# Kernel optimization log

Measured on AMD Instinct MI355X. Metric: run time of the kernel, lower is better.

## Reference

```python
import jax, jax.numpy as jnp
from jax import lax
import numpy as np

HIDDEN = 1024
FEAT = 512
PREV = 10
PRED = 20
BATCH = 1024


def setup_inputs() -> dict:
    key = jax.random.key(0)
    ks = jax.random.split(key, 12)
    s_in = 1.0 / np.sqrt(FEAT)
    s_h = 1.0 / np.sqrt(HIDDEN)
    return {
        "real_input": jax.random.normal(ks[0], (BATCH, PREV + PRED, FEAT), jnp.float32),
        "fake_input": jax.random.normal(ks[1], (BATCH, PRED, FEAT), jnp.float32),
        "Wx": jax.random.normal(ks[2], (FEAT, 4 * HIDDEN), jnp.float32) * s_in,
        "Wh": jax.random.normal(ks[3], (HIDDEN, 4 * HIDDEN), jnp.float32) * s_h,
        "b": jnp.zeros((4 * HIDDEN,), jnp.float32),
        "w2": jax.random.normal(ks[4], (HIDDEN, 1), jnp.float32) * s_h,
        "b2": jnp.zeros((1,), jnp.float32),
        "w3": jax.random.normal(ks[5], (1, 1), jnp.float32),
        "b3": jnp.zeros((1,), jnp.float32),
        "w4": jax.random.normal(ks[6], (1, 1), jnp.float32),
        "b4": jnp.zeros((1,), jnp.float32),
    }


def _lstm_hidden_states(seq, Wx, Wh, b):
    # seq: [B, T, F] -> hidden states hs: [T, B, H]
    B = seq.shape[0]
    xz = jnp.einsum("btf,fk->btk", seq, Wx) + b  # precompute input projections

    def step(carry, xz_t):
        h, c = carry
        z = xz_t + h @ Wh  # [B, 4H]
        i, f, g, o = jnp.split(z, 4, axis=-1)
        i = jax.nn.sigmoid(i)
        f = jax.nn.sigmoid(f)
        g = jnp.tanh(g)
        o = jax.nn.sigmoid(o)
        c = f * c + i * g
        h = o * jnp.tanh(c)
        return (h, c), h

    h0 = jnp.zeros((B, Wh.shape[0]), seq.dtype)
    _, hs = lax.scan(step, (h0, h0), jnp.swapaxes(xz, 0, 1))
    return hs


def _dense_chain(h, w2, b2, w3, b3, w4, b4):
    x = jnp.tanh(h @ w2 + b2)
    x = jnp.tanh(x @ w3 + b3)
    x = jnp.tanh(x @ w4 + b4)
    return x


def reference(real_input, fake_input, Wx, Wh, b, w2, b2, w3, b3, w4, b4):
    # trajectory_real[k] is the prefix real_input[:, :PREV+k+1]; running the
    # LSTM from zero state over each prefix equals taking hidden state at
    # step PREV+k of a single scan over the full sequence.
    fake_seq = jnp.concatenate([real_input[:, :PREV, :], fake_input], axis=1)

    hs_real = _lstm_hidden_states(real_input, Wx, Wh, b)[PREV:PREV + PRED]  # [PRED,B,H]
    hs_fake = _lstm_hidden_states(fake_seq, Wx, Wh, b)[PREV:PREV + PRED]

    real_pred = _dense_chain(hs_real, w2, b2, w3, b3, w4, b4)  # [PRED,B,1]
    fake_pred = _dense_chain(hs_fake, w2, b2, w3, b3, w4, b4)

    real_pred = jnp.swapaxes(real_pred, 0, 1)  # [B,PRED,1]
    fake_pred = jnp.swapaxes(fake_pred, 0, 1)
    return real_pred, fake_pred
```

## Files before the change

kernel.cpp:

```cpp
#include <hip/hip_runtime.h>
#include <hip/hip_bf16.h>
#include <stdint.h>
#include <string.h>

#define HIDDEN 1024
#define FEAT   512
#define PREV   10
#define PRED   20
#define BATCH  1024
#define KTOT   (HIDDEN + FEAT)
#define N4H    4096
#define TSTEPS (PREV + PRED)
#define NBLK   256
#define NTHR   512
#define NKT    24
#define TILEB  16384

typedef __attribute__((ext_vector_type(8))) short short8;
typedef __attribute__((ext_vector_type(4))) float f32x4;
typedef unsigned long long ull;

typedef __attribute__((address_space(3))) unsigned int u32_lds;
typedef const __attribute__((address_space(1))) unsigned int u32_gbl;

__device__ __forceinline__ void async16(void* lds, const void* g) {
  u32_lds* lp = (u32_lds*)(unsigned int)(uintptr_t)lds;
  u32_gbl* gp = (u32_gbl*)(uintptr_t)g;
  __builtin_amdgcn_global_load_lds(gp, lp, 16, 0, 0);
}

__device__ __forceinline__ float sigmoidf_(float x) {
  return 1.0f / (1.0f + __expf(-x));
}
__device__ __forceinline__ float tanhf_(float x) {
  return 1.0f - 2.0f / (1.0f + __expf(2.0f * x));
}

__device__ __forceinline__ ull cload(const void* p) {
  return __hip_atomic_load((const ull*)p, __ATOMIC_RELAXED, __HIP_MEMORY_SCOPE_AGENT);
}
__device__ __forceinline__ void cstore(void* p, ull v) {
  __hip_atomic_store((ull*)p, v, __ATOMIC_RELAXED, __HIP_MEMORY_SCOPE_AGENT);
}
__device__ __forceinline__ float cload4(const void* p) {
  return __hip_atomic_load((const float*)p, __ATOMIC_RELAXED, __HIP_MEMORY_SCOPE_AGENT);
}
__device__ __forceinline__ void cstore4(void* p, float v) {
  __hip_atomic_store((float*)p, v, __ATOMIC_RELAXED, __HIP_MEMORY_SCOPE_AGENT);
}

__global__ void pack_w_kernel(const float* __restrict__ Wx, const float* __restrict__ Wh,
                              __hip_bfloat16* __restrict__ WpT) {
  __shared__ float tile[64][65];
  const int k0 = blockIdx.x * 64, n0 = blockIdx.y * 64;
  const int tid = threadIdx.x;
  const float* src = (k0 < HIDDEN) ? (Wh + (size_t)k0 * N4H) : (Wx + (size_t)(k0 - HIDDEN) * N4H);
  {
    const int jl = tid & 15, g = (tid >> 4) & 3, klb = tid >> 6;
#pragma unroll
    for (int it = 0; it < 16; ++it) {
      int kl = klb + it * 4;
      tile[kl][4 * jl + g] = src[(size_t)kl * N4H + g * HIDDEN + (n0 >> 2) + jl];
    }
  }
  __syncthreads();
  {
    const int kl = tid & 63, nlb = tid >> 6;
#pragma unroll
    for (int it = 0; it < 16; ++it) {
      int nl = nlb + it * 4;
      WpT[(size_t)(n0 + nl) * KTOT + k0 + kl] = __float2bfloat16(tile[kl][nl]);
    }
  }
}

__global__ void pack_wf_kernel(const __hip_bfloat16* __restrict__ WpT,
                               __hip_bfloat16* __restrict__ Wf) {
  int id = blockIdx.x * 256 + threadIdx.x;
  if (id >= (N4H / 16) * (KTOT / 32) * 64) return;
  int l = id & 63, fg = id >> 6;
  int kg = fg % (KTOT / 32), ng = fg / (KTOT / 32);
  int n = ng * 16 + (l & 15);
  int k0 = kg * 32 + (l >> 4) * 8;
  *(short8*)(Wf + (size_t)id * 8) = *(const short8*)(WpT + (size_t)n * KTOT + k0);
}

__global__ void pack_bias_kernel(const float* __restrict__ b, float* __restrict__ bp) {
  int n = blockIdx.x * 256 + threadIdx.x;
  if (n < N4H) bp[n] = b[(n & 3) * HIDDEN + (n >> 2)];
}

__global__ void cvt_x_kernel(const float* __restrict__ xr, const float* __restrict__ xf,
                             __hip_bfloat16* __restrict__ xrb, __hip_bfloat16* __restrict__ xfb) {
  const int NR4 = BATCH * TSTEPS * FEAT / 4;
  const int NF4 = BATCH * PRED * FEAT / 4;
  int i = blockIdx.x * 256 + threadIdx.x;
  float4 v;
  __hip_bfloat16* dst;
  if (i < NR4) {
    v = ((const float4*)xr)[i];
    dst = xrb + (size_t)i * 4;
  } else {
    int j = i - NR4;
    if (j >= NF4) return;
    v = ((const float4*)xf)[j];
    dst = xfb + (size_t)j * 4;
  }
  dst[0] = __float2bfloat16(v.x);
  dst[1] = __float2bfloat16(v.y);
  dst[2] = __float2bfloat16(v.z);
  dst[3] = __float2bfloat16(v.w);
}

__global__ __launch_bounds__(512, 2)
void lstm_persistent(const __hip_bfloat16* __restrict__ xrb,
                     const __hip_bfloat16* __restrict__ xfb,
                     const __hip_bfloat16* __restrict__ Wf,
                     const float* __restrict__ biasp,
                     const float* __restrict__ w2,
                     __hip_bfloat16* __restrict__ hb0,
                     __hip_bfloat16* __restrict__ hb1,
                     float* __restrict__ cbuf,
                     float* __restrict__ accout,
                     unsigned* __restrict__ bar) {
  __shared__ __align__(16) char smem[2 * TILEB + 128 * 68 * 2];

  const int tid = threadIdx.x;
  const int bid = blockIdx.x;
  const int nt = bid & 15, rt = bid >> 4;
  const int n0 = nt * 256;
  const int r0 = rt * 128;
  const int w = tid >> 6, l = tid & 63;
  const int sub = l >> 3;
  const int csrc = (l & 7) ^ sub;
  const int quad = l >> 4, lrow = l & 15;
  const int wn = w & 3, wb = w >> 2;
  unsigned* cnt = bar;
  unsigned* flag = bar + 32;
  unsigned short* hT = (unsigned short*)(smem + 2 * TILEB);

  const char* wfL = (const char*)Wf + ((size_t)(nt * 16 + wn * 4) * (KTOT / 32)) * 1024 + (size_t)l * 16;
  const int ldsW = (w * 16 + sub) * 128 + (l & 7) * 16;

  float w2r[4];
#pragma unroll
  for (int mi = 0; mi < 4; ++mi) w2r[mi] = w2[nt * 64 + wn * 16 + mi * 4 + quad];

  float creg[16];
#pragma unroll
  for (int i = 0; i < 16; ++i) creg[i] = 0.f;

  short8 wSA[8], wSB[8];
  ull sd0, sd1, sd2, sd3;

#define ISSUE_W(S, WS)                                                                 \
  do {                                                                                 \
    if ((S) < NKT) {                                                                   \
      const char* _wp = wfL + (size_t)(S) * 2048;                                      \
      _Pragma("unroll")                                                                \
      for (int _mi = 0; _mi < 4; ++_mi)                                                \
        _Pragma("unroll")                                                              \
        for (int _kk = 0; _kk < 2; ++_kk)                                              \
          WS[_mi * 2 + _kk] =                                                          \
              *(const short8*)(_wp + _mi * ((KTOT / 32) * 1024) + _kk * 1024);         \
    }                                                                                  \
  } while (0)

#define STAGE_ISSUE(S)                                                                 \
  do {                                                                                 \
    if ((S) < 16) {                                                                    \
      sd0 = cload(hsA0 + (size_t)(S) * 64);                                            \
      sd1 = cload(hsA0 + (size_t)(S) * 64 + 4);                                        \
      sd2 = cload(hsA1 + (size_t)(S) * 64);                                            \
      sd3 = cload(hsA1 + (size_t)(S) * 64 + 4);                                        \
    } else if ((S) < NKT) {                                                            \
      char* _sb = smem + ((S) & 1) * TILEB;                                            \
      async16(_sb + (w * 16) * 128,     xA0 + (size_t)((S) * 64 - HIDDEN));            \
      async16(_sb + (w * 16 + 8) * 128, xA1 + (size_t)((S) * 64 - HIDDEN));            \
    }                                                                                  \
  } while (0)

#define STAGE_WRITE(S)                                                                 \
  do {                                                                                 \
    if ((S) < 16) {                                                                    \
      ull* _lw = (ull*)(smem + ((S) & 1) * TILEB + ldsW);                              \
      _lw[0] = sd0;                                                                    \
      _lw[1] = sd1;                                                                    \
      ull* _lw2 = (ull*)(smem + ((S) & 1) * TILEB + ldsW + 1024);                      \
      _lw2[0] = sd2;                                                                   \
      _lw2[1] = sd3;                                                                   \
    }                                                                                  \
  } while (0)

#define KT_COMPUTE(KT, WS)                                                             \
  do {                                                                                 \
    const char* _cb = smem + ((KT) & 1) * TILEB;                                       \
    _Pragma("unroll")                                                                  \
    for (int kk = 0; kk < 2; ++kk) {                                                   \
      const int swz = (((kk << 2) + quad) ^ (lrow & 7)) * 16;                          \
      short8 bf[4];                                                                    \
      _Pragma("unroll")                                                                \
      for (int bi = 0; bi < 4; ++bi)                                                   \
        bf[bi] = *(const short8*)(_cb + (wb * 64 + bi * 16 + lrow) * 128 + swz);       \
      _Pragma("unroll")                                                                \
      for (int mi = 0; mi < 4; ++mi)                                                   \
        _Pragma("unroll")                                                              \
        for (int bi = 0; bi < 4; ++bi)                                                 \
          acc[mi][bi] = __builtin_amdgcn_mfma_f32_16x16x32_bf16(WS[mi * 2 + kk],       \
                            bf[bi], acc[mi][bi], 0, 0, 0);                             \
    }                                                                                  \
  } while (0)

#define KT_BODY(KT, WSc, WSn)                                                          \
  do {                                                                                 \
    STAGE_ISSUE((KT) + 1);                                                             \
    ISSUE_W((KT) + 1, WSn);                                                            \
    KT_COMPUTE(KT, WSc);                                                               \
    STAGE_WRITE((KT) + 1);                                                             \
    __syncthreads();                                                                   \
  } while (0)

#pragma unroll 1
  for (int t = 0; t < TSTEPS; ++t) {
    const unsigned short* hcur = (const unsigned short*)((t & 1) ? hb1 : hb0);
    unsigned short* hnx = (unsigned short*)((t & 1) ? hb0 : hb1);
    const bool active = (t >= PREV) || (rt < 8);

    if (active) {
      if (t == PREV && r0 >= BATCH) {
#pragma unroll
        for (int mi = 0; mi < 4; ++mi)
#pragma unroll
          for (int bi = 0; bi < 4; ++bi)
            creg[mi * 4 + bi] = cload4(&cbuf[(size_t)(r0 - BATCH + wb * 64 + bi * 16 + lrow) * HIDDEN
                                             + nt * 64 + wn * 16 + mi * 4 + quad]);
      }
      const int r0h = (t == PREV && r0 >= BATCH) ? (r0 - BATCH) : r0;

      const unsigned short* hsA0 = hcur + (size_t)(r0h + w * 16 + sub) * HIDDEN + csrc * 8;
      const unsigned short* hsA1 = hsA0 + 8 * HIDDEN;
      const unsigned short* xb;
      size_t xstr;
      if (r0 < BATCH) {
        xb = (const unsigned short*)xrb + ((size_t)r0 * TSTEPS + t) * FEAT;
        xstr = (size_t)TSTEPS * FEAT;
      } else {
        xb = (const unsigned short*)xfb + ((size_t)(r0 - BATCH) * PRED + (t - PREV)) * FEAT;
        xstr = (size_t)PRED * FEAT;
      }
      const unsigned short* xA0 = xb + (w * 16 + sub) * xstr + csrc * 8;
      const unsigned short* xA1 = xA0 + 8 * xstr;

      f32x4 acc[4][4];
#pragma unroll
      for (int a = 0; a < 4; ++a)
#pragma unroll
        for (int b_ = 0; b_ < 4; ++b_) acc[a][b_] = (f32x4){0.f, 0.f, 0.f, 0.f};

      STAGE_ISSUE(0);
      if (t == 0) ISSUE_W(0, wSA);
      STAGE_WRITE(0);
      __syncthreads();

#pragma unroll 1
      for (int m2 = 0; m2 < NKT / 2; ++m2) {
        const int kt = 2 * m2;
        KT_BODY(kt, wSA, wSB);
        KT_BODY(kt + 1, wSB, wSA);
      }

      const int kout = t - PREV;
      float psum[4] = {0.f, 0.f, 0.f, 0.f};
#pragma unroll
      for (int mi = 0; mi < 4; ++mi) {
        const float4 bi4 = *(const float4*)&biasp[n0 + wn * 64 + mi * 16 + quad * 4];
#pragma unroll
        for (int bi = 0; bi < 4; ++bi) {
          f32x4 z = acc[mi][bi];
          float gi = sigmoidf_(z[0] + bi4.x);
          float gf = sigmoidf_(z[1] + bi4.y);
          float gg = tanhf_(z[2] + bi4.z);
          float go = sigmoidf_(z[3] + bi4.w);
          const int ci = mi * 4 + bi;
          float cnew = gf * creg[ci] + gi * gg;
          float hnew = go * tanhf_(cnew);
          creg[ci] = cnew;
          __hip_bfloat16 hbv = __float2bfloat16(hnew);
          hT[(wb * 64 + bi * 16 + lrow) * 68 + wn * 16 + mi * 4 + quad] =
              *(unsigned short*)&hbv;
          if (t >= PREV) psum[bi] += hnew * w2r[mi];
          if (t == PREV - 1)
            cstore4(&cbuf[(size_t)(r0 + wb * 64 + bi * 16 + lrow) * HIDDEN
                          + nt * 64 + wn * 16 + mi * 4 + quad], cnew);
        }
      }
      __syncthreads();
      {
        const int er = tid >> 2, ejq = tid & 3;
#pragma unroll
        for (int it = 0; it < 4; ++it) {
          int jl = ejq * 16 + it * 4;
          ull v;
          memcpy(&v, &hT[er * 68 + jl], 8);
          cstore(hnx + (size_t)(r0 + er) * HIDDEN + nt * 64 + jl, v);
        }
      }
      if (t >= PREV) {
#pragma unroll
        for (int bi = 0; bi < 4; ++bi) {
          float v = psum[bi];
          v += __shfl_down(v, 32);
          v += __shfl_down(v, 16);
          if (quad == 0)
            atomicAdd(&accout[(size_t)(r0 + wb * 64 + bi * 16 + lrow) * PRED + kout], v);
        }
      }
    }

    if (t < TSTEPS - 1) {
      const bool nact = (t + 1 >= PREV) || (rt < 8);
      if (nact) ISSUE_W(0, wSA);
      __syncthreads();
      if (tid == 0) {
        unsigned ph = (unsigned)(t + 1);
        unsigned old = __hip_atomic_fetch_add(cnt, 1u, __ATOMIC_RELAXED, __HIP_MEMORY_SCOPE_AGENT);
        if (old == NBLK - 1) {
          __hip_atomic_store(cnt, 0u, __ATOMIC_RELAXED, __HIP_MEMORY_SCOPE_AGENT);
          __hip_atomic_store(flag, ph, __ATOMIC_RELAXED, __HIP_MEMORY_SCOPE_AGENT);
        } else {
          while (__hip_atomic_load(flag, __ATOMIC_RELAXED, __HIP_MEMORY_SCOPE_AGENT) < ph)
            __builtin_amdgcn_s_sleep(4);
        }
      }
      __syncthreads();
    }
  }
#undef ISSUE_W
#undef STAGE_ISSUE
#undef STAGE_WRITE
#undef KT_COMPUTE
#undef KT_BODY
}

__global__ void final_kernel(const float* __restrict__ accout, const float* __restrict__ b2,
                             const float* __restrict__ w3, const float* __restrict__ b3,
                             const float* __restrict__ w4, const float* __restrict__ b4,
                             float* __restrict__ out) {
  int i = blockIdx.x * 256 + threadIdx.x;
  const int half = BATCH * PRED;
  if (i >= 2 * half) return;
  int r, k;
  if (i < half) {
    r = i / PRED;
    k = i % PRED;
  } else {
    r = BATCH + (i - half) / PRED;
    k = (i - half) % PRED;
  }
  float x = tanhf_(accout[r * PRED + k] + b2[0]);
  x = tanhf_(x * w3[0] + b3[0]);
  x = tanhf_(x * w4[0] + b4[0]);
  out[i] = x;
}

extern "C" void kernel_launch(void* const* d_in, const int* in_sizes, int n_in,
                              void* d_out, int out_size, void* d_ws, size_t ws_size,
                              hipStream_t stream) {
  const float* real_input = (const float*)d_in[0];
  const float* fake_input = (const float*)d_in[1];
  const float* Wx = (const float*)d_in[2];
  const float* Wh = (const float*)d_in[3];
  const float* b  = (const float*)d_in[4];
  const float* w2 = (const float*)d_in[5];
  const float* b2 = (const float*)d_in[6];
  const float* w3 = (const float*)d_in[7];
  const float* b3 = (const float*)d_in[8];
  const float* w4 = (const float*)d_in[9];
  const float* b4 = (const float*)d_in[10];
  float* out = (float*)d_out;

  char* ws = (char*)d_ws;
  size_t off = 0;
  __hip_bfloat16* Wf = (__hip_bfloat16*)(ws + off);   off += (size_t)N4H * KTOT * 2;
  float* biasp = (float*)(ws + off);                  off += (size_t)N4H * 4;
  __hip_bfloat16* hb0 = (__hip_bfloat16*)(ws + off);  off += (size_t)2 * BATCH * HIDDEN * 2;
  __hip_bfloat16* hb1 = (__hip_bfloat16*)(ws + off);  off += (size_t)2 * BATCH * HIDDEN * 2;
  float* cbuf = (float*)(ws + off);                   off += (size_t)BATCH * HIDDEN * 4;
  float* accout = (float*)(ws + off);                 off += (size_t)2 * BATCH * PRED * 4;
  unsigned* bar = (unsigned*)(ws + off);              off += 256;
  __hip_bfloat16* xrb = (__hip_bfloat16*)(ws + off);
  __hip_bfloat16* WpT = (__hip_bfloat16*)(ws + off);  off += (size_t)BATCH * TSTEPS * FEAT * 2;
  __hip_bfloat16* xfb = (__hip_bfloat16*)(ws + off);  off += (size_t)BATCH * PRED * FEAT * 2;

  hipMemsetAsync(hb0, 0, (size_t)2 * BATCH * HIDDEN * 2, stream);
  hipMemsetAsync(accout, 0, (size_t)2 * BATCH * PRED * 4, stream);
  hipMemsetAsync(bar, 0, 256, stream);

  pack_w_kernel<<<dim3(KTOT / 64, N4H / 64), 256, 0, stream>>>(Wx, Wh, WpT);
  pack_bias_kernel<<<N4H / 256, 256, 0, stream>>>(b, biasp);
  pack_wf_kernel<<<((N4H / 16) * (KTOT / 32) * 64 + 255) / 256, 256, 0, stream>>>(WpT, Wf);
  {
    int n4 = BATCH * TSTEPS * FEAT / 4 + BATCH * PRED * FEAT / 4;
    cvt_x_kernel<<<(n4 + 255) / 256, 256, 0, stream>>>(real_input, fake_input, xrb, xfb);
  }

  {
    const __hip_bfloat16* a_xrb = xrb;
    const __hip_bfloat16* a_xfb = xfb;
    const __hip_bfloat16* a_Wf = Wf;
    const float* a_biasp = biasp;
    const float* a_w2 = w2;
    __hip_bfloat16* a_hb0 = hb0;
    __hip_bfloat16* a_hb1 = hb1;
    float* a_cbuf = cbuf;
    float* a_acc = accout;
    unsigned* a_bar = bar;
    void* args[10] = {&a_xrb, &a_xfb, &a_Wf, &a_biasp, &a_w2,
                      &a_hb0, &a_hb1, &a_cbuf, &a_acc, &a_bar};
    hipError_t e = hipLaunchCooperativeKernel((const void*)lstm_persistent,
                                              dim3(NBLK), dim3(NTHR), args, 0, stream);
    if (e != hipSuccess) {
      lstm_persistent<<<dim3(NBLK), dim3(NTHR), 0, stream>>>(
          xrb, xfb, Wf, biasp, w2, hb0, hb1, cbuf, accout, bar);
    }
  }

  final_kernel<<<(2 * BATCH * PRED + 255) / 256, 256, 0, stream>>>(accout, b2, w3, b3, w4, b4, out);
}
```

Baseline: 1.401 ms.

## Store h and x in MFMA-fragment layout, load B operands directly to registers

Adds a per-timestep buffer that holds both the hidden state and the bf16 inputs already in the MFMA B-fragment layout. Each block now loads weight and activation fragments straight from global memory into registers with a register double-buffer, which removes the LDS staging, async copies and most __syncthreads in the inner K loop. The epilogue writes new h directly in fragment layout for the next step. In exchange it uses more global memory (a buffer for every timestep), depends on L2 to serve the B-fragment reloads, and drops the prefetch of weights across the grid barrier.

```diff
diff --git a/kernel.cpp b/kernel.cpp
--- a/kernel.cpp
+++ b/kernel.cpp
@@ -14,31 +14,26 @@
 #define NBLK   256
 #define NTHR   512
 #define NKT    24
-#define TILEB  16384
+#define NKG    (KTOT / 32)
+#define STEPB  ((size_t)128 * NKG * 1024)
 
 typedef __attribute__((ext_vector_type(8))) short short8;
 typedef __attribute__((ext_vector_type(4))) float f32x4;
 typedef unsigned long long ull;
 
-typedef __attribute__((address_space(3))) unsigned int u32_lds;
-typedef const __attribute__((address_space(1))) unsigned int u32_gbl;
-
-__device__ __forceinline__ void async16(void* lds, const void* g) {
-  u32_lds* lp = (u32_lds*)(unsigned int)(uintptr_t)lds;
-  u32_gbl* gp = (u32_gbl*)(uintptr_t)g;
-  __builtin_amdgcn_global_load_lds(gp, lp, 16, 0, 0);
-}
-
 __device__ __forceinline__ float sigmoidf_(float x) {
   return 1.0f / (1.0f + __expf(-x));
 }
 __device__ __forceinline__ float tanhf_(float x) {
   return 1.0f - 2.0f / (1.0f + __expf(2.0f * x));
 }
-
-__device__ __forceinline__ ull cload(const void* p) {
-  return __hip_atomic_load((const ull*)p, __ATOMIC_RELAXED, __HIP_MEMORY_SCOPE_AGENT);
-}
+__device__ __forceinline__ unsigned short f2bf(float x) {
+  __hip_bfloat16 h = __float2bfloat16(x);
+  unsigned short u;
+  memcpy(&u, &h, 2);
+  return u;
+}
+
 __device__ __forceinline__ void cstore(void* p, ull v) {
   __hip_atomic_store((ull*)p, v, __ATOMIC_RELAXED, __HIP_MEMORY_SCOPE_AGENT);
 }
@@ -77,9 +72,9 @@
 __global__ void pack_wf_kernel(const __hip_bfloat16* __restrict__ WpT,
                                __hip_bfloat16* __restrict__ Wf) {
   int id = blockIdx.x * 256 + threadIdx.x;
-  if (id >= (N4H / 16) * (KTOT / 32) * 64) return;
+  if (id >= (N4H / 16) * NKG * 64) return;
   int l = id & 63, fg = id >> 6;
-  int kg = fg % (KTOT / 32), ng = fg / (KTOT / 32);
+  int kg = fg % NKG, ng = fg / NKG;
   int n = ng * 16 + (l & 15);
   int k0 = kg * 32 + (l >> 4) * 8;
   *(short8*)(Wf + (size_t)id * 8) = *(const short8*)(WpT + (size_t)n * KTOT + k0);
@@ -90,40 +85,54 @@
   if (n < N4H) bp[n] = b[(n & 3) * HIDDEN + (n >> 2)];
 }
 
-__global__ void cvt_x_kernel(const float* __restrict__ xr, const float* __restrict__ xf,
-                             __hip_bfloat16* __restrict__ xrb, __hip_bfloat16* __restrict__ xfb) {
-  const int NR4 = BATCH * TSTEPS * FEAT / 4;
-  const int NF4 = BATCH * PRED * FEAT / 4;
-  int i = blockIdx.x * 256 + threadIdx.x;
-  float4 v;
-  __hip_bfloat16* dst;
-  if (i < NR4) {
-    v = ((const float4*)xr)[i];
-    dst = xrb + (size_t)i * 4;
+__global__ void pack_bx_kernel(const float* __restrict__ xr, const float* __restrict__ xf,
+                               char* __restrict__ bF) {
+  const int REALF = 64 * TSTEPS * 16;
+  const int FAKEF = 64 * PRED * 16;
+  int id = blockIdx.x * 256 + threadIdx.x;
+  int fid = id >> 6, l = id & 63;
+  if (fid >= REALF + FAKEF) return;
+  const float* src;
+  int bg, t, kgx;
+  if (fid < REALF) {
+    kgx = fid & 15;
+    int r = fid >> 4;
+    t = r % TSTEPS;
+    bg = r / TSTEPS;
+    src = xr + ((size_t)(bg * 16 + (l & 15)) * TSTEPS + t) * FEAT + kgx * 32 + (l >> 4) * 8;
   } else {
-    int j = i - NR4;
-    if (j >= NF4) return;
-    v = ((const float4*)xf)[j];
-    dst = xfb + (size_t)j * 4;
-  }
-  dst[0] = __float2bfloat16(v.x);
-  dst[1] = __float2bfloat16(v.y);
-  dst[2] = __float2bfloat16(v.z);
-  dst[3] = __float2bfloat16(v.w);
+    int f2 = fid - REALF;
+    kgx = f2 & 15;
+    int r = f2 >> 4;
+    int tf = r % PRED;
+    int bg2 = r / PRED;
+    t = PREV + tf;
+    bg = 64 + bg2;
+    src = xf + ((size_t)(bg2 * 16 + (l & 15)) * PRED + tf) * FEAT + kgx * 32 + (l >> 4) * 8;
+  }
+  float4 v0 = *(const float4*)src;
+  float4 v1 = *(const float4*)(src + 4);
+  short8 o;
+  o[0] = (short)f2bf(v0.x);
+  o[1] = (short)f2bf(v0.y);
+  o[2] = (short)f2bf(v0.z);
+  o[3] = (short)f2bf(v0.w);
+  o[4] = (short)f2bf(v1.x);
+  o[5] = (short)f2bf(v1.y);
+  o[6] = (short)f2bf(v1.z);
+  o[7] = (short)f2bf(v1.w);
+  *(short8*)(bF + (size_t)t * STEPB + (((size_t)bg * NKG + 32 + kgx) << 10) + l * 16) = o;
 }
 
 __global__ __launch_bounds__(512, 2)
-void lstm_persistent(const __hip_bfloat16* __restrict__ xrb,
-                     const __hip_bfloat16* __restrict__ xfb,
+void lstm_persistent(char* __restrict__ bF,
                      const __hip_bfloat16* __restrict__ Wf,
                      const float* __restrict__ biasp,
                      const float* __restrict__ w2,
-                     __hip_bfloat16* __restrict__ hb0,
-                     __hip_bfloat16* __restrict__ hb1,
                      float* __restrict__ cbuf,
                      float* __restrict__ accout,
                      unsigned* __restrict__ bar) {
-  __shared__ __align__(16) char smem[2 * TILEB + 128 * 68 * 2];
+  __shared__ __align__(16) unsigned short hT[128 * 68];
 
   const int tid = threadIdx.x;
   const int bid = blockIdx.x;
@@ -131,16 +140,12 @@
   const int n0 = nt * 256;
   const int r0 = rt * 128;
   const int w = tid >> 6, l = tid & 63;
-  const int sub = l >> 3;
-  const int csrc = (l & 7) ^ sub;
   const int quad = l >> 4, lrow = l & 15;
   const int wn = w & 3, wb = w >> 2;
   unsigned* cnt = bar;
   unsigned* flag = bar + 32;
-  unsigned short* hT = (unsigned short*)(smem + 2 * TILEB);
-
-  const char* wfL = (const char*)Wf + ((size_t)(nt * 16 + wn * 4) * (KTOT / 32)) * 1024 + (size_t)l * 16;
-  const int ldsW = (w * 16 + sub) * 128 + (l & 7) * 16;
+
+  const char* wfL = (const char*)Wf + ((size_t)(nt * 16 + wn * 4) * NKG) * 1024 + (size_t)l * 16;
 
   float w2r[4];
 #pragma unroll
@@ -150,80 +155,41 @@
 #pragma unroll
   for (int i = 0; i < 16; ++i) creg[i] = 0.f;
 
-  short8 wSA[8], wSB[8];
-  ull sd0, sd1, sd2, sd3;
-
-#define ISSUE_W(S, WS)                                                                 \
+#define LOADA(S, WS)                                                                   \
   do {                                                                                 \
-    if ((S) < NKT) {                                                                   \
-      const char* _wp = wfL + (size_t)(S) * 2048;                                      \
+    _Pragma("unroll")                                                                  \
+    for (int _mi = 0; _mi < 4; ++_mi)                                                  \
+      _Pragma("unroll")                                                                \
+      for (int _kk = 0; _kk < 2; ++_kk)                                                \
+        WS[_mi * 2 + _kk] = *(const short8*)(wfL + (size_t)_mi * (NKG * 1024) +        \
+                                             (((size_t)(S) * 2 + _kk) << 10));         \
+  } while (0)
+
+#define LOADB(S, HS)                                                                   \
+  do {                                                                                 \
+    const char* _b = ((S) < 16) ? bLh : bLx;                                           \
+    _Pragma("unroll")                                                                  \
+    for (int _bi = 0; _bi < 4; ++_bi)                                                  \
+      _Pragma("unroll")                                                                \
+      for (int _kk = 0; _kk < 2; ++_kk)                                                \
+        HS[_bi * 2 + _kk] = *(const short8*)(_b + (size_t)_bi * (NKG * 1024) +         \
+                                             (((size_t)(S) * 2 + _kk) << 10));         \
+  } while (0)
+
+#define COMP(WS, HS)                                                                   \
+  do {                                                                                 \
+    _Pragma("unroll")                                                                  \
+    for (int _kk = 0; _kk < 2; ++_kk)                                                  \
       _Pragma("unroll")                                                                \
       for (int _mi = 0; _mi < 4; ++_mi)                                                \
         _Pragma("unroll")                                                              \
-        for (int _kk = 0; _kk < 2; ++_kk)                                              \
-          WS[_mi * 2 + _kk] =                                                          \
-              *(const short8*)(_wp + _mi * ((KTOT / 32) * 1024) + _kk * 1024);         \
-    }                                                                                  \
-  } while (0)
-
-#define STAGE_ISSUE(S)                                                                 \
-  do {                                                                                 \
-    if ((S) < 16) {                                                                    \
-      sd0 = cload(hsA0 + (size_t)(S) * 64);                                            \
-      sd1 = cload(hsA0 + (size_t)(S) * 64 + 4);                                        \
-      sd2 = cload(hsA1 + (size_t)(S) * 64);                                            \
-      sd3 = cload(hsA1 + (size_t)(S) * 64 + 4);                                        \
-    } else if ((S) < NKT) {                                                            \
-      char* _sb = smem + ((S) & 1) * TILEB;                                            \
-      async16(_sb + (w * 16) * 128,     xA0 + (size_t)((S) * 64 - HIDDEN));            \
-      async16(_sb + (w * 16 + 8) * 128, xA1 + (size_t)((S) * 64 - HIDDEN));            \
-    }                                                                                  \
-  } while (0)
-
-#define STAGE_WRITE(S)                                                                 \
-  do {                                                                                 \
-    if ((S) < 16) {                                                                    \
-      ull* _lw = (ull*)(smem + ((S) & 1) * TILEB + ldsW);                              \
-      _lw[0] = sd0;                                                                    \
-      _lw[1] = sd1;                                                                    \
-      ull* _lw2 = (ull*)(smem + ((S) & 1) * TILEB + ldsW + 1024);                      \
-      _lw2[0] = sd2;                                                                   \
-      _lw2[1] = sd3;                                                                   \
-    }                                                                                  \
-  } while (0)
-
-#define KT_COMPUTE(KT, WS)                                                             \
-  do {                                                                                 \
-    const char* _cb = smem + ((KT) & 1) * TILEB;                                       \
-    _Pragma("unroll")                                                                  \
-    for (int kk = 0; kk < 2; ++kk) {                                                   \
-      const int swz = (((kk << 2) + quad) ^ (lrow & 7)) * 16;                          \
-      short8 bf[4];                                                                    \
-      _Pragma("unroll")                                                                \
-      for (int bi = 0; bi < 4; ++bi)                                                   \
-        bf[bi] = *(const short8*)(_cb + (wb * 64 + bi * 16 + lrow) * 128 + swz);       \
-      _Pragma("unroll")                                                                \
-      for (int mi = 0; mi < 4; ++mi)                                                   \
-        _Pragma("unroll")                                                              \
-        for (int bi = 0; bi < 4; ++bi)                                                 \
-          acc[mi][bi] = __builtin_amdgcn_mfma_f32_16x16x32_bf16(WS[mi * 2 + kk],       \
-                            bf[bi], acc[mi][bi], 0, 0, 0);                             \
-    }                                                                                  \
-  } while (0)
-
-#define KT_BODY(KT, WSc, WSn)                                                          \
-  do {                                                                                 \
-    STAGE_ISSUE((KT) + 1);                                                             \
-    ISSUE_W((KT) + 1, WSn);                                                            \
-    KT_COMPUTE(KT, WSc);                                                               \
-    STAGE_WRITE((KT) + 1);                                                             \
-    __syncthreads();                                                                   \
+        for (int _bi = 0; _bi < 4; ++_bi)                                              \
+          acc[_mi][_bi] = __builtin_amdgcn_mfma_f32_16x16x32_bf16(                     \
+              WS[_mi * 2 + _kk], HS[_bi * 2 + _kk], acc[_mi][_bi], 0, 0, 0);           \
   } while (0)
 
 #pragma unroll 1
   for (int t = 0; t < TSTEPS; ++t) {
-    const unsigned short* hcur = (const unsigned short*)((t & 1) ? hb1 : hb0);
-    unsigned short* hnx = (unsigned short*)((t & 1) ? hb0 : hb1);
     const bool active = (t >= PREV) || (rt < 8);
 
     if (active) {
@@ -237,19 +203,9 @@
       }
       const int r0h = (t == PREV && r0 >= BATCH) ? (r0 - BATCH) : r0;
 
-      const unsigned short* hsA0 = hcur + (size_t)(r0h + w * 16 + sub) * HIDDEN + csrc * 8;
-      const unsigned short* hsA1 = hsA0 + 8 * HIDDEN;
-      const unsigned short* xb;
-      size_t xstr;
-      if (r0 < BATCH) {
-        xb = (const unsigned short*)xrb + ((size_t)r0 * TSTEPS + t) * FEAT;
-        xstr = (size_t)TSTEPS * FEAT;
-      } else {
-        xb = (const unsigned short*)xfb + ((size_t)(r0 - BATCH) * PRED + (t - PREV)) * FEAT;
-        xstr = (size_t)PRED * FEAT;
-      }
-      const unsigned short* xA0 = xb + (w * 16 + sub) * xstr + csrc * 8;
-      const unsigned short* xA1 = xA0 + 8 * xstr;
+      const char* bT = bF + (size_t)t * STEPB;
+      const char* bLh = bT + (((size_t)((r0h >> 4) + wb * 4) * NKG) << 10) + (size_t)l * 16;
+      const char* bLx = bT + (((size_t)((r0  >> 4) + wb * 4) * NKG) << 10) + (size_t)l * 16;
 
       f32x4 acc[4][4];
 #pragma unroll
@@ -257,16 +213,19 @@
 #pragma unroll
         for (int b_ = 0; b_ < 4; ++b_) acc[a][b_] = (f32x4){0.f, 0.f, 0.f, 0.f};
 
-      STAGE_ISSUE(0);
-      if (t == 0) ISSUE_W(0, wSA);
-      STAGE_WRITE(0);
-      __syncthreads();
-
+      short8 wA[8], hB[8], wA2[8], hB2[8];
+      LOADA(0, wA);
+      LOADB(0, hB);
 #pragma unroll 1
-      for (int m2 = 0; m2 < NKT / 2; ++m2) {
-        const int kt = 2 * m2;
-        KT_BODY(kt, wSA, wSB);
-        KT_BODY(kt + 1, wSB, wSA);
+      for (int kt = 0; kt < NKT; kt += 2) {
+        LOADA(kt + 1, wA2);
+        LOADB(kt + 1, hB2);
+        COMP(wA, hB);
+        if (kt + 2 < NKT) {
+          LOADA(kt + 2, wA);
+          LOADB(kt + 2, hB);
+        }
+        COMP(wA2, hB2);
       }
 
       const int kout = t - PREV;
@@ -285,24 +244,28 @@
           float cnew = gf * creg[ci] + gi * gg;
           float hnew = go * tanhf_(cnew);
           creg[ci] = cnew;
-          __hip_bfloat16 hbv = __float2bfloat16(hnew);
-          hT[(wb * 64 + bi * 16 + lrow) * 68 + wn * 16 + mi * 4 + quad] =
-              *(unsigned short*)&hbv;
+          hT[(wb * 64 + bi * 16 + lrow) * 68 + wn * 16 + mi * 4 + quad] = f2bf(hnew);
           if (t >= PREV) psum[bi] += hnew * w2r[mi];
           if (t == PREV - 1)
             cstore4(&cbuf[(size_t)(r0 + wb * 64 + bi * 16 + lrow) * HIDDEN
                           + nt * 64 + wn * 16 + mi * 4 + quad], cnew);
         }
       }
-      __syncthreads();
-      {
-        const int er = tid >> 2, ejq = tid & 3;
-#pragma unroll
-        for (int it = 0; it < 4; ++it) {
-          int jl = ejq * 16 + it * 4;
-          ull v;
-          memcpy(&v, &hT[er * 68 + jl], 8);
-          cstore(hnx + (size_t)(r0 + er) * HIDDEN + nt * 64 + jl, v);
+      if (t + 1 < TSTEPS) {
+        __syncthreads();
+        char* bT1 = bF + (size_t)(t + 1) * STEPB;
+#pragma unroll
+        for (int pass = 0; pass < 2; ++pass) {
+          int s = tid + pass * 512;
+          int f = s >> 6, lq = s & 63;
+          int bgl = f >> 1, kgl = f & 1;
+          int br = bgl * 16 + (lq & 15);
+          int jb = kgl * 32 + (lq >> 4) * 8;
+          ull d0 = *(const ull*)&hT[br * 68 + jb];
+          ull d1 = *(const ull*)&hT[br * 68 + jb + 4];
+          char* dst = bT1 + (((size_t)((r0 >> 4) + bgl) * NKG + nt * 2 + kgl) << 10) + lq * 16;
+          cstore(dst, d0);
+          cstore(dst + 8, d1);
         }
       }
       if (t >= PREV) {
@@ -318,8 +281,6 @@
     }
 
     if (t < TSTEPS - 1) {
-      const bool nact = (t + 1 >= PREV) || (rt < 8);
-      if (nact) ISSUE_W(0, wSA);
       __syncthreads();
       if (tid == 0) {
         unsigned ph = (unsigned)(t + 1);
@@ -335,11 +296,9 @@
       __syncthreads();
     }
   }
-#undef ISSUE_W
-#undef STAGE_ISSUE
-#undef STAGE_WRITE
-#undef KT_COMPUTE
-#undef KT_BODY
+#undef LOADA
+#undef LOADB
+#undef COMP
 }
 
 __global__ void final_kernel(const float* __restrict__ accout, const float* __restrict__ b2,
@@ -383,45 +342,38 @@
   size_t off = 0;
   __hip_bfloat16* Wf = (__hip_bfloat16*)(ws + off);   off += (size_t)N4H * KTOT * 2;
   float* biasp = (float*)(ws + off);                  off += (size_t)N4H * 4;
-  __hip_bfloat16* hb0 = (__hip_bfloat16*)(ws + off);  off += (size_t)2 * BATCH * HIDDEN * 2;
-  __hip_bfloat16* hb1 = (__hip_bfloat16*)(ws + off);  off += (size_t)2 * BATCH * HIDDEN * 2;
   float* cbuf = (float*)(ws + off);                   off += (size_t)BATCH * HIDDEN * 4;
   float* accout = (float*)(ws + off);                 off += (size_t)2 * BATCH * PRED * 4;
-  unsigned* bar = (unsigned*)(ws + off);              off += 256;
-  __hip_bfloat16* xrb = (__hip_bfloat16*)(ws + off);
-  __hip_bfloat16* WpT = (__hip_bfloat16*)(ws + off);  off += (size_t)BATCH * TSTEPS * FEAT * 2;
-  __hip_bfloat16* xfb = (__hip_bfloat16*)(ws + off);  off += (size_t)BATCH * PRED * FEAT * 2;
-
-  hipMemsetAsync(hb0, 0, (size_t)2 * BATCH * HIDDEN * 2, stream);
+  unsigned* bar = (unsigned*)(ws + off);              off += 1024;
+  char* bF = ws + off;                                off += (size_t)TSTEPS * STEPB;
+  __hip_bfloat16* WpT = (__hip_bfloat16*)(bF + (size_t)28 * STEPB);
+
+  hipMemsetAsync(bF, 0, STEPB, stream);
   hipMemsetAsync(accout, 0, (size_t)2 * BATCH * PRED * 4, stream);
-  hipMemsetAsync(bar, 0, 256, stream);
+  hipMemsetAsync(bar, 0, 1024, stream);
 
   pack_w_kernel<<<dim3(KTOT / 64, N4H / 64), 256, 0, stream>>>(Wx, Wh, WpT);
   pack_bias_kernel<<<N4H / 256, 256, 0, stream>>>(b, biasp);
-  pack_wf_kernel<<<((N4H / 16) * (KTOT / 32) * 64 + 255) / 256, 256, 0, stream>>>(WpT, Wf);
+  pack_wf_kernel<<<((N4H / 16) * NKG * 64 + 255) / 256, 256, 0, stream>>>(WpT, Wf);
   {
-    int n4 = BATCH * TSTEPS * FEAT / 4 + BATCH * PRED * FEAT / 4;
-    cvt_x_kernel<<<(n4 + 255) / 256, 256, 0, stream>>>(real_input, fake_input, xrb, xfb);
+    int nthr = (64 * TSTEPS * 16 + 64 * PRED * 16) * 64;
+    pack_bx_kernel<<<(nthr + 255) / 256, 256, 0, stream>>>(real_input, fake_input, bF);
   }
 
   {
-    const __hip_bfloat16* a_xrb = xrb;
-    const __hip_bfloat16* a_xfb = xfb;
+    char* a_bF = bF;
     const __hip_bfloat16* a_Wf = Wf;
     const float* a_biasp = biasp;
     const float* a_w2 = w2;
-    __hip_bfloat16* a_hb0 = hb0;
-    __hip_bfloat16* a_hb1 = hb1;
     float* a_cbuf = cbuf;
     float* a_acc = accout;
     unsigned* a_bar = bar;
-    void* args[10] = {&a_xrb, &a_xfb, &a_Wf, &a_biasp, &a_w2,
-                      &a_hb0, &a_hb1, &a_cbuf, &a_acc, &a_bar};
+    void* args[7] = {&a_bF, &a_Wf, &a_biasp, &a_w2, &a_cbuf, &a_acc, &a_bar};
     hipError_t e = hipLaunchCooperativeKernel((const void*)lstm_persistent,
                                               dim3(NBLK), dim3(NTHR), args, 0, stream);
     if (e != hipSuccess) {
       lstm_persistent<<<dim3(NBLK), dim3(NTHR), 0, stream>>>(
-          xrb, xfb, Wf, biasp, w2, hb0, hb1, cbuf, accout, bar);
+          bF, Wf, biasp, w2, cbuf, accout, bar);
     }
   }
 
```

New measurement: 1.361 ms. -2.9%, faster.
